# Optimization experiments

Measured on AMD Instinct MI355X. Metric: run time of the kernel, lower is better.

The kernel has to match this reference:

```python
import jax, jax.numpy as jnp
import numpy as np

B, S, D = 32, 256, 128
K = 16          # num_sample (negatives + the positive appended last)
V = 50000       # vocab / num_classes


def setup_inputs() -> dict:
    key = jax.random.key(0)
    k1, k2, k3, k4 = jax.random.split(key, 4)
    return {
        "input_latent": jax.random.normal(k1, (B, S, D), dtype=jnp.float32),
        "target_labels": jax.random.randint(k2, (B, S), 0, V, dtype=jnp.int64),
        "batch_samples": jax.random.randint(k3, (B, S * (K - 1)), 0, V, dtype=jnp.int64),
        "embed_weight": jax.random.normal(k4, (V, D), dtype=jnp.float32),
    }


def reference(input_latent, target_labels, batch_samples, embed_weight):
    b, s, d = input_latent.shape
    out_emb = embed_weight[target_labels]                      # [B,S,D] positives
    neg_emb = embed_weight[batch_samples].reshape(b, s, K - 1, d)
    # Candidates per target position j: K-1 negatives + the positive itself (last)
    samples = jnp.concatenate([neg_emb, out_emb[:, :, None, :]], axis=2)  # [B,S,K,D]
    # sample_rep[b,i,j,k] = latent[b,i] . samples[b,j,k]
    sample_scores = jnp.einsum('bid,bjkd->bijk', input_latent, samples)   # [B,S,S,K]
    # output_rep[b,i,j] = latent[b,i] . out_emb[b,j] (== sample_scores[...,K-1])
    out_scores = jnp.einsum('bid,bjd->bij', input_latent, out_emb)        # [B,S,S]
    # log( exp(out - max) / sum_k exp(sample - max) ) = out - logsumexp(sample)
    lse = jax.scipy.special.logsumexp(sample_scores, axis=3)              # [B,S,S]
    return out_scores - lse
```

## Files before the change

### kernel.cpp

```cpp
#include <hip/hip_runtime.h>
#include <hip/hip_bf16.h>
#include <math.h>

#define BB 32
#define SS 256
#define DD 128
#define KK 16
#define VV 50000
#define SK (SS*KK)

typedef __attribute__((ext_vector_type(8))) short bf16x8;
typedef __attribute__((ext_vector_type(4))) float f32x4;
typedef __attribute__((ext_vector_type(16))) float f32x16;
typedef unsigned short ushort_t;

static __device__ __forceinline__ short f2bf(float f) {
    unsigned u = __float_as_uint(f);
    unsigned r = (u + 0x7fffu + ((u >> 16) & 1u)) >> 16;
    return (short)r;
}

static __device__ __forceinline__ int lds_off(int row, int d) {
    return row * 256 + ((d * 2) ^ ((row & 15) << 4));
}

static __device__ __forceinline__ void gload_lds16(const void* g, void* lds) {
    __builtin_amdgcn_global_load_lds(
        (const __attribute__((address_space(1))) unsigned int*)g,
        (__attribute__((address_space(3))) unsigned int*)lds, 16, 0, 0);
}

#define NLAT (BB*SS*DD)
#define NCHUNK_LAT (NLAT/8)

__global__ __launch_bounds__(256)
void convert_lat_kernel(const float* __restrict__ latent,
                        ushort_t* __restrict__ ws_lat)
{
    int i = blockIdx.x * 256 + threadIdx.x;
    if (i >= NCHUNK_LAT) return;
    const float* src = latent + (size_t)i * 8;
    float f[8];
    *(float4*)(f + 0) = ((const float4*)src)[0];
    *(float4*)(f + 4) = ((const float4*)src)[1];
    short o[8];
    #pragma unroll
    for (int e = 0; e < 8; ++e) o[e] = f2bf(f[e]);
    *(bf16x8*)(ws_lat + (size_t)i * 8) = *(bf16x8*)o;
}

#define MT 64
#define NT 128

__global__ __launch_bounds__(256)
void neg_loss_main(const ushort_t* __restrict__ lat_bf,
                   const int*      __restrict__ labels,
                   const int*      __restrict__ samples,
                   const float*    __restrict__ embed,
                   float* __restrict__ out)
{
    __shared__ char ldsA[2][MT * 256];

    const int b    = blockIdx.z;
    const int n0   = blockIdx.x * NT;
    const int tid  = threadIdx.x;
    const int wave = tid >> 6;
    const int lane = tid & 63;
    const int q    = lane & 15;
    const int sub  = lane >> 4;
    const int l31  = lane & 31;
    const int hi   = lane >> 5;

    const int rB  = wave * 32 + l31;
    const int gc  = n0 + rB;
    const int j   = gc >> 4;
    const int k   = gc & 15;
    const int idx = (k < 15)
        ? samples[(size_t)b * (SS * (KK - 1)) + j * (KK - 1) + k]
        : labels[b * SS + j];

    #pragma unroll
    for (int t = 0; t < 4; ++t) {
        const int r0 = wave * 16 + t * 4;
        const int r  = r0 + sub;
        const ushort_t* src = lat_bf + ((size_t)(b * SS + r) * DD)
                                     + ((q ^ (r & 15)) << 3);
        gload_lds16(src, ldsA[0] + r0 * 256);
    }

    const float* rowp = embed + (size_t)idx * DD + hi * 8;
    f32x4 fb[16];
    #pragma unroll
    for (int ks = 0; ks < 8; ++ks) {
        fb[2 * ks]     = *(const f32x4*)(rowp + ks * 16);
        fb[2 * ks + 1] = *(const f32x4*)(rowp + ks * 16 + 4);
    }
    bf16x8 av[8];
    #pragma unroll
    for (int ks = 0; ks < 8; ++ks) {
        short t8[8];
        #pragma unroll
        for (int e = 0; e < 4; ++e) t8[e]     = f2bf(fb[2 * ks][e]);
        #pragma unroll
        for (int e = 0; e < 4; ++e) t8[4 + e] = f2bf(fb[2 * ks + 1][e]);
        av[ks] = *(bf16x8*)t8;
    }

    __syncthreads();

    const int jb = (n0 >> 4) + wave * 2;

    for (int mt = 0; mt < 4; ++mt) {
        const int cur = mt & 1;

        if (mt < 3) {
            #pragma unroll
            for (int t = 0; t < 4; ++t) {
                const int r0 = wave * 16 + t * 4;
                const int r  = r0 + sub;
                const ushort_t* src = lat_bf
                    + ((size_t)(b * SS + ((mt + 1) * MT + r)) * DD)
                    + ((q ^ (r & 15)) << 3);
                gload_lds16(src, ldsA[cur ^ 1] + r0 * 256);
            }
        }

        f32x16 acc0 = {}, acc1 = {};
        #pragma unroll
        for (int ks = 0; ks < 8; ++ks) {
            const int d = ks * 16 + hi * 8;
            bf16x8 bv0 = *(const bf16x8*)(ldsA[cur] + lds_off(l31, d));
            bf16x8 bv1 = *(const bf16x8*)(ldsA[cur] + lds_off(32 + l31, d));
            acc0 = __builtin_amdgcn_mfma_f32_32x32x16_bf16(av[ks], bv0, acc0, 0, 0, 0);
            acc1 = __builtin_amdgcn_mfma_f32_32x32x16_bf16(av[ks], bv1, acc1, 0, 0, 0);
        }

        #pragma unroll
        for (int f = 0; f < 2; ++f) {
            const f32x16 v = f ? acc1 : acc0;
            float pm0 = fmaxf(fmaxf(fmaxf(v[0], v[1]), fmaxf(v[2], v[3])),
                              fmaxf(fmaxf(v[4], v[5]), fmaxf(v[6], v[7])));
            float pm1 = fmaxf(fmaxf(fmaxf(v[8], v[9]), fmaxf(v[10], v[11])),
                              fmaxf(fmaxf(v[12], v[13]), fmaxf(v[14], v[15])));
            float om0 = fmaxf(pm0, __shfl_xor(pm0, 32));
            float om1 = fmaxf(pm1, __shfl_xor(pm1, 32));
            float ps0 = __expf(v[0] - om0) + __expf(v[1] - om0)
                      + __expf(v[2] - om0) + __expf(v[3] - om0)
                      + __expf(v[4] - om0) + __expf(v[5] - om0)
                      + __expf(v[6] - om0) + __expf(v[7] - om0);
            float ps1 = __expf(v[8]  - om1) + __expf(v[9]  - om1)
                      + __expf(v[10] - om1) + __expf(v[11] - om1)
                      + __expf(v[12] - om1) + __expf(v[13] - om1)
                      + __expf(v[14] - om1) + __expf(v[15] - om1);
            float s0 = ps0 + __shfl_xor(ps0, 32);
            float s1 = ps1 + __shfl_xor(ps1, 32);
            float pos0 = __shfl_xor(v[7], 32);
            float pos1 = v[15];
            const float pos = hi ? pos1 : pos0;
            const float om  = hi ? om1  : om0;
            const float s   = hi ? s1   : s0;
            const int i = mt * MT + f * 32 + l31;
            out[((size_t)b * SS + i) * SS + (jb + hi)] = pos - om - __logf(s);
        }

        __syncthreads();
    }
}

__global__ __launch_bounds__(256)
void neg_loss_fallback(const float* __restrict__ latent,
                       const int*   __restrict__ labels,
                       const int*   __restrict__ samples,
                       const float* __restrict__ embed,
                       float* __restrict__ out)
{
    __shared__ char ldsA[64 * 256];
    __shared__ char ldsB[64 * 256];

    const int b   = blockIdx.z;
    const int m0  = blockIdx.y * 64;
    const int n0  = blockIdx.x * 64;
    const int tid = threadIdx.x;

    {
        const int r  = tid >> 2;
        const int d0 = (tid & 3) * 32;
        const float* src = latent + ((size_t)b * SS + (m0 + r)) * DD + d0;
        float f[32];
        #pragma unroll
        for (int c = 0; c < 8; ++c)
            *(float4*)(f + 4 * c) = ((const float4*)src)[c];
        #pragma unroll
        for (int c = 0; c < 4; ++c) {
            short tmp[8];
            #pragma unroll
            for (int e = 0; e < 8; ++e) tmp[e] = f2bf(f[c * 8 + e]);
            *(bf16x8*)(ldsA + lds_off(r, d0 + c * 8)) = *(bf16x8*)tmp;
        }
    }
    {
        const int c   = tid >> 2;
        const int d0  = (tid & 3) * 32;
        const int col = n0 + c;
        const int j   = col >> 4;
        const int k   = col & 15;
        const int idx = (k < 15) ? samples[(size_t)b * (SS * (KK - 1)) + j * (KK - 1) + k]
                                 : labels[b * SS + j];
        const float* src = embed + (size_t)idx * DD + d0;
        float f[32];
        #pragma unroll
        for (int cc = 0; cc < 8; ++cc)
            *(float4*)(f + 4 * cc) = ((const float4*)src)[cc];
        #pragma unroll
        for (int cc = 0; cc < 4; ++cc) {
            short tmp[8];
            #pragma unroll
            for (int e = 0; e < 8; ++e) tmp[e] = f2bf(f[cc * 8 + e]);
            *(bf16x8*)(ldsB + lds_off(c, d0 + cc * 8)) = *(bf16x8*)tmp;
        }
    }
    __syncthreads();

    const int wave = tid >> 6;
    const int lane = tid & 63;
    const int wm = wave >> 1, wn = wave & 1;
    const int lr = lane & 15;
    const int lk = (lane >> 4) * 8;
    const int sub = lane >> 4;

    f32x4 acc[2][2] = {};
    #pragma unroll
    for (int ks = 0; ks < 4; ++ks) {
        const int d = ks * 32 + lk;
        bf16x8 a[2], bb2[2];
        #pragma unroll
        for (int mf = 0; mf < 2; ++mf)
            a[mf] = *(const bf16x8*)(ldsA + lds_off(wm * 32 + mf * 16 + lr, d));
        #pragma unroll
        for (int nf = 0; nf < 2; ++nf)
            bb2[nf] = *(const bf16x8*)(ldsB + lds_off(wn * 32 + nf * 16 + lr, d));
        #pragma unroll
        for (int mf = 0; mf < 2; ++mf)
            #pragma unroll
            for (int nf = 0; nf < 2; ++nf)
                acc[mf][nf] = __builtin_amdgcn_mfma_f32_16x16x32_bf16(
                    bb2[nf], a[mf], acc[mf][nf], 0, 0, 0);
    }

    #pragma unroll
    for (int mf = 0; mf < 2; ++mf) {
        #pragma unroll
        for (int nf = 0; nf < 2; ++nf) {
            const f32x4 v = acc[mf][nf];
            float mx = fmaxf(fmaxf(v[0], v[1]), fmaxf(v[2], v[3]));
            mx = fmaxf(mx, __shfl_xor(mx, 16));
            mx = fmaxf(mx, __shfl_xor(mx, 32));
            float e = __expf(v[0] - mx) + __expf(v[1] - mx)
                    + __expf(v[2] - mx) + __expf(v[3] - mx);
            e += __shfl_xor(e, 16);
            e += __shfl_xor(e, 32);
            float pos = __shfl(v[3], (lane & 15) | 48);
            if (sub == 0) {
                const int i  = m0 + wm * 32 + mf * 16 + (lane & 15);
                const int jj = (n0 >> 4) + wn * 2 + nf;
                out[((size_t)b * SS + i) * SS + jj] = pos - mx - __logf(e);
            }
        }
    }
}

extern "C" void kernel_launch(void* const* d_in, const int* in_sizes, int n_in,
                              void* d_out, int out_size, void* d_ws, size_t ws_size,
                              hipStream_t stream) {
    const float* latent  = (const float*)d_in[0];
    const int*   labels  = (const int*)d_in[1];
    const int*   samples = (const int*)d_in[2];
    const float* embed   = (const float*)d_in[3];
    float* out = (float*)d_out;

    const size_t ws_needed = (size_t)NLAT * 2;
    if (ws_size >= ws_needed) {
        ushort_t* ws_lat = (ushort_t*)d_ws;
        convert_lat_kernel<<<(NCHUNK_LAT + 255) / 256, 256, 0, stream>>>(
            latent, ws_lat);
        dim3 grid(SK / NT, 1, BB);
        neg_loss_main<<<grid, dim3(256), 0, stream>>>(
            ws_lat, labels, samples, embed, out);
    } else {
        dim3 grid(SK / 64, SS / 64, BB);
        neg_loss_fallback<<<grid, dim3(256), 0, stream>>>(
            latent, labels, samples, embed, out);
    }
}
```

Before: 35.62 us.

## Split latent rows across grid y, drop double-buffered loop and barriers

The main kernel now splits the 256 latent rows into two 128-row halves across blockIdx.y. Each block loads its half into LDS once and runs two unrolled compute tiles, replacing the four-step double-buffered loop with per-iteration barriers. This doubles the grid for more parallelism and sets an occupancy hint through launch_bounds. The cost is that every embedding row is gathered and converted twice, once per half. The bf16 conversion now uses the library intrinsic, and the exp sum is reassociated into a tree.

```diff
diff --git a/kernel.cpp b/kernel.cpp
--- a/kernel.cpp
+++ b/kernel.cpp
@@ -15,9 +15,8 @@
 typedef unsigned short ushort_t;
 
 static __device__ __forceinline__ short f2bf(float f) {
-    unsigned u = __float_as_uint(f);
-    unsigned r = (u + 0x7fffu + ((u >> 16) & 1u)) >> 16;
-    return (short)r;
+    __hip_bfloat16 h = __float2bfloat16(f);
+    return *(short*)&h;
 }
 
 static __device__ __forceinline__ int lds_off(int row, int d) {
@@ -49,19 +48,20 @@
     *(bf16x8*)(ws_lat + (size_t)i * 8) = *(bf16x8*)o;
 }
 
-#define MT 64
-#define NT 128
-
-__global__ __launch_bounds__(256)
+#define MTB 128
+#define NT  128
+
+__global__ __launch_bounds__(256, 5)
 void neg_loss_main(const ushort_t* __restrict__ lat_bf,
                    const int*      __restrict__ labels,
                    const int*      __restrict__ samples,
                    const float*    __restrict__ embed,
                    float* __restrict__ out)
 {
-    __shared__ char ldsA[2][MT * 256];
+    __shared__ char ldsA[MTB * 256];
 
     const int b    = blockIdx.z;
+    const int m0   = blockIdx.y * MTB;
     const int n0   = blockIdx.x * NT;
     const int tid  = threadIdx.x;
     const int wave = tid >> 6;
@@ -71,6 +71,15 @@
     const int l31  = lane & 31;
     const int hi   = lane >> 5;
 
+    #pragma unroll
+    for (int t = 0; t < 8; ++t) {
+        const int r0 = wave * 32 + t * 4;
+        const int r  = r0 + sub;
+        const ushort_t* src = lat_bf + ((size_t)(b * SS + m0 + r) * DD)
+                                     + ((q ^ (r & 15)) << 3);
+        gload_lds16(src, ldsA + r0 * 256);
+    }
+
     const int rB  = wave * 32 + l31;
     const int gc  = n0 + rB;
     const int j   = gc >> 4;
@@ -79,15 +88,6 @@
         ? samples[(size_t)b * (SS * (KK - 1)) + j * (KK - 1) + k]
         : labels[b * SS + j];
 
-    #pragma unroll
-    for (int t = 0; t < 4; ++t) {
-        const int r0 = wave * 16 + t * 4;
-        const int r  = r0 + sub;
-        const ushort_t* src = lat_bf + ((size_t)(b * SS + r) * DD)
-                                     + ((q ^ (r & 15)) << 3);
-        gload_lds16(src, ldsA[0] + r0 * 256);
-    }
-
     const float* rowp = embed + (size_t)idx * DD + hi * 8;
     f32x4 fb[16];
     #pragma unroll
@@ -110,27 +110,14 @@
 
     const int jb = (n0 >> 4) + wave * 2;
 
-    for (int mt = 0; mt < 4; ++mt) {
-        const int cur = mt & 1;
-
-        if (mt < 3) {
-            #pragma unroll
-            for (int t = 0; t < 4; ++t) {
-                const int r0 = wave * 16 + t * 4;
-                const int r  = r0 + sub;
-                const ushort_t* src = lat_bf
-                    + ((size_t)(b * SS + ((mt + 1) * MT + r)) * DD)
-                    + ((q ^ (r & 15)) << 3);
-                gload_lds16(src, ldsA[cur ^ 1] + r0 * 256);
-            }
-        }
-
+    #pragma unroll
+    for (int mt = 0; mt < 2; ++mt) {
         f32x16 acc0 = {}, acc1 = {};
         #pragma unroll
         for (int ks = 0; ks < 8; ++ks) {
             const int d = ks * 16 + hi * 8;
-            bf16x8 bv0 = *(const bf16x8*)(ldsA[cur] + lds_off(l31, d));
-            bf16x8 bv1 = *(const bf16x8*)(ldsA[cur] + lds_off(32 + l31, d));
+            bf16x8 bv0 = *(const bf16x8*)(ldsA + lds_off(mt * 64 + l31, d));
+            bf16x8 bv1 = *(const bf16x8*)(ldsA + lds_off(mt * 64 + 32 + l31, d));
             acc0 = __builtin_amdgcn_mfma_f32_32x32x16_bf16(av[ks], bv0, acc0, 0, 0, 0);
             acc1 = __builtin_amdgcn_mfma_f32_32x32x16_bf16(av[ks], bv1, acc1, 0, 0, 0);
         }
@@ -144,26 +131,24 @@
                               fmaxf(fmaxf(v[12], v[13]), fmaxf(v[14], v[15])));
             float om0 = fmaxf(pm0, __shfl_xor(pm0, 32));
             float om1 = fmaxf(pm1, __shfl_xor(pm1, 32));
-            float ps0 = __expf(v[0] - om0) + __expf(v[1] - om0)
-                      + __expf(v[2] - om0) + __expf(v[3] - om0)
-                      + __expf(v[4] - om0) + __expf(v[5] - om0)
-                      + __expf(v[6] - om0) + __expf(v[7] - om0);
-            float ps1 = __expf(v[8]  - om1) + __expf(v[9]  - om1)
-                      + __expf(v[10] - om1) + __expf(v[11] - om1)
-                      + __expf(v[12] - om1) + __expf(v[13] - om1)
-                      + __expf(v[14] - om1) + __expf(v[15] - om1);
-            float s0 = ps0 + __shfl_xor(ps0, 32);
-            float s1 = ps1 + __shfl_xor(ps1, 32);
+            float e0 = ((__expf(v[0] - om0) + __expf(v[1] - om0))
+                      + (__expf(v[2] - om0) + __expf(v[3] - om0)))
+                     + ((__expf(v[4] - om0) + __expf(v[5] - om0))
+                      + (__expf(v[6] - om0) + __expf(v[7] - om0)));
+            float e1 = ((__expf(v[8]  - om1) + __expf(v[9]  - om1))
+                      + (__expf(v[10] - om1) + __expf(v[11] - om1)))
+                     + ((__expf(v[12] - om1) + __expf(v[13] - om1))
+                      + (__expf(v[14] - om1) + __expf(v[15] - om1)));
+            float s0 = e0 + __shfl_xor(e0, 32);
+            float s1 = e1 + __shfl_xor(e1, 32);
             float pos0 = __shfl_xor(v[7], 32);
             float pos1 = v[15];
             const float pos = hi ? pos1 : pos0;
             const float om  = hi ? om1  : om0;
             const float s   = hi ? s1   : s0;
-            const int i = mt * MT + f * 32 + l31;
+            const int i = m0 + mt * 64 + f * 32 + l31;
             out[((size_t)b * SS + i) * SS + (jb + hi)] = pos - om - __logf(s);
         }
-
-        __syncthreads();
     }
 }
 
@@ -283,7 +268,7 @@
         ushort_t* ws_lat = (ushort_t*)d_ws;
         convert_lat_kernel<<<(NCHUNK_LAT + 255) / 256, 256, 0, stream>>>(
             latent, ws_lat);
-        dim3 grid(SK / NT, 1, BB);
+        dim3 grid(SK / NT, SS / MTB, BB);
         neg_loss_main<<<grid, dim3(256), 0, stream>>>(
             ws_lat, labels, samples, embed, out);
     } else {
```

After: 36.92 us. 3.7% more time.
